# Optimization experiments

Measured on AMD Instinct MI355X. Metric: run time of the kernel, lower is better.

Reference implementation:

```python
import jax, jax.numpy as jnp
import numpy as np
from jax import lax

IN_C, OUT_C, K, Z_DIM, STRIDE = 128, 128, 3, 256, 1


def setup_inputs() -> dict:
    key = jax.random.key(0)
    k1, k2, k3, k4, k5 = jax.random.split(key, 5)
    B, H, W = 16, 64, 64
    x = jax.random.normal(k1, (B, IN_C, H, W), dtype=jnp.float32)
    z = jax.random.normal(k2, (B, Z_DIM), dtype=jnp.float32)
    # base conv weight, He-style init as in the torch module
    base_weight = jax.random.normal(k3, (OUT_C, IN_C, K, K), dtype=jnp.float32) * (2.0 / (IN_C * K * K)) ** 0.5
    # delta_weight_head: nn.Linear(z_dim, out_c*in_c*k*k) -> weight [out_dim, z_dim], bias [out_dim]
    out_dim = OUT_C * IN_C * K * K
    lim = 1.0 / np.sqrt(Z_DIM)
    head_w = jax.random.uniform(k4, (out_dim, Z_DIM), dtype=jnp.float32, minval=-lim, maxval=lim)
    head_b = jax.random.uniform(k5, (out_dim,), dtype=jnp.float32, minval=-lim, maxval=lim)
    return {"x": x, "z": z, "base_weight": base_weight, "head_w": head_w, "head_b": head_b}


def reference(x, z, base_weight, head_w, head_b):
    B = x.shape[0]
    # per-sample weight deltas: [B, out_c*in_c*k*k] -> [B, out_c, in_c, k, k]
    delta_w = (z @ head_w.T + head_b).reshape(B, OUT_C, IN_C, K, K)
    w = base_weight[None] + delta_w  # [B, out_c, in_c, k, k]
    pad = K // 2

    def conv_one(xb, wb):
        # xb: [in_c, H, W], wb: [out_c, in_c, k, k]
        return lax.conv_general_dilated(
            xb[None], wb, window_strides=(STRIDE, STRIDE),
            padding=[(pad, pad), (pad, pad)],
            dimension_numbers=("NCHW", "OIHW", "NCHW"))[0]

    out = jax.vmap(conv_one)(x, w)  # [B, out_c, H_out, W_out]
    return out
```

## Files before the change

### kernel.cpp

```cpp
#include <hip/hip_runtime.h>
#include <cstdint>
#include <cstddef>

typedef _Float16 f16;
typedef _Float16 f16x8 __attribute__((ext_vector_type(8)));
typedef _Float16 f16x4 __attribute__((ext_vector_type(4)));
typedef float f32x4 __attribute__((ext_vector_type(4)));

#define BATCH 16
#define INC   128
#define OUTC  128
#define HH    64
#define WW    64
#define HP    66
#define WP    66
#define ZDIM  256

#define XP_ELEMS (16ull * HP * WP * INC)
#define WA_ELEMS (16ull * 9 * OUTC * INC)

#define GLOAD16(g, l)                                                     \
    __builtin_amdgcn_global_load_lds(                                     \
        (const __attribute__((address_space(1))) void*)(g),               \
        (__attribute__((address_space(3))) void*)(l), 16, 0, 0)

__device__ __forceinline__ f16x8 cvt8(float4 a, float4 b) {
    f16x8 r;
    r[0] = (f16)a.x; r[1] = (f16)a.y; r[2] = (f16)a.z; r[3] = (f16)a.w;
    r[4] = (f16)b.x; r[5] = (f16)b.y; r[6] = (f16)b.z; r[7] = (f16)b.w;
    return r;
}

__global__ __launch_bounds__(256) void prep(const float* __restrict__ x,
                                            const float* __restrict__ z,
                                            const float* __restrict__ base_w,
                                            const float* __restrict__ head_w,
                                            const float* __restrict__ head_b,
                                            f16* __restrict__ xp,
                                            f16* __restrict__ wA) {
    __shared__ float tile[32 * 65];
    int blk = blockIdx.x;
    int tid = threadIdx.x;

    if (blk < 2304) {
        int lane = tid & 63;
        int wv   = tid >> 6;
        int r16  = lane & 15;
        int quad = lane >> 4;
        int tl   = blk * 4 + wv;
        int icb  = tl & 7;
        int oc   = (tl >> 3) & 127;
        int r    = tl >> 10;
        int base = (oc * 128 + icb * 16) * 9 + r;
        int myrow = base + 9 * r16;

        const float4* zrow = (const float4*)(z + (size_t)r16 * ZDIM);
        f16x8 bfr[8];
#pragma unroll
        for (int s = 0; s < 8; ++s)
            bfr[s] = cvt8(zrow[s * 8 + quad * 2], zrow[s * 8 + quad * 2 + 1]);

        const float4* hw = (const float4*)(head_w + (size_t)myrow * ZDIM);
        float4 a[3][2];
        a[0][0] = hw[quad * 2];     a[0][1] = hw[quad * 2 + 1];
        a[1][0] = hw[8 + quad * 2]; a[1][1] = hw[8 + quad * 2 + 1];
        f32x4 acc = {0.f, 0.f, 0.f, 0.f};
#pragma unroll
        for (int s = 0; s < 8; ++s) {
            if (s + 2 < 8) {
                a[(s + 2) % 3][0] = hw[(s + 2) * 8 + quad * 2];
                a[(s + 2) % 3][1] = hw[(s + 2) * 8 + quad * 2 + 1];
            }
            acc = __builtin_amdgcn_mfma_f32_16x16x32_f16(
                cvt8(a[s % 3][0], a[s % 3][1]), bfr[s], acc, 0, 0, 0);
        }

        f16x4 ov;
        int icl = quad * 4;
#pragma unroll
        for (int reg = 0; reg < 4; ++reg) {
            int o = base + 9 * (icl + reg);
            ov[reg] = (f16)(base_w[o] + head_b[o] + acc[reg]);
        }
        size_t idx = (((size_t)r16 * 9 + r) * OUTC + oc) * INC + icb * 16 + icl;
        *(f16x4*)(wA + idx) = ov;

    } else if (blk < 6400) {
        int xb  = blk - 2304;
        int icC = xb & 3;
        int h   = (xb >> 2) & 63;
        int b   = xb >> 8;
        int ic0 = icC * 32;
        {
            int i = tid >> 3;
            int j = tid & 7;
            const float4* src = (const float4*)(x + (((size_t)b * INC + ic0 + i) * HH + h) * WW) + j * 2;
            float4 v0 = src[0];
            float4 v1 = src[1];
            float* tp = tile + i * 65 + j * 8;
            tp[0] = v0.x; tp[1] = v0.y; tp[2] = v0.z; tp[3] = v0.w;
            tp[4] = v1.x; tp[5] = v1.y; tp[6] = v1.z; tp[7] = v1.w;
        }
        __syncthreads();
        {
            int w = tid >> 2;
            int q = tid & 3;
            f16 o8[8];
#pragma unroll
            for (int jj = 0; jj < 8; ++jj)
                o8[jj] = (f16)tile[(q * 8 + jj) * 65 + w];
            f16* dst = xp + (((size_t)b * HP + (h + 1)) * WP + (w + 1)) * INC + ic0 + q * 8;
            *(uint4*)dst = *(uint4*)o8;
        }

    } else {
        unsigned i = (unsigned)(blk - 6400) * 256u + (unsigned)tid;
        unsigned b = i / 4160;
        unsigned j = i - b * 4160;
        unsigned row, wc, ic8;
        if (j < 2112) {
            row = (j < 1056) ? 0u : 65u;
            unsigned jj = (j < 1056) ? j : j - 1056;
            wc  = jj >> 4;
            ic8 = jj & 15;
        } else {
            unsigned j2 = j - 2112;
            row = 1 + (j2 >> 5);
            unsigned k = j2 & 31;
            wc  = (k < 16) ? 0u : 65u;
            ic8 = k & 15;
        }
        uint4 zv = {0u, 0u, 0u, 0u};
        *(uint4*)(xp + (((size_t)b * HP + row) * WP + wc) * INC + ic8 * 8) = zv;
    }
}

__global__ __launch_bounds__(256) void conv(const f16* __restrict__ xp,
                                            const f16* __restrict__ wA,
                                            float* __restrict__ out) {
    int blk0 = blockIdx.x;
    int blk  = (blk0 & 7) * 64 + (blk0 >> 3);
    int b  = blk >> 5;
    int pt = blk & 31;
    int h0 = pt * 2;

    int tid    = threadIdx.x;
    int lane   = tid & 63;
    int wv     = tid >> 6;
    int ocHalf = wv & 1;
    int pHalf  = wv >> 1;
    int m0     = ocHalf * 64;
    int row16  = lane & 15;
    int quad   = lane >> 4;

    __shared__ __align__(16) f16 ws0[3 * 128 * 32];
    __shared__ __align__(16) f16 ws1[3 * 128 * 32];
    __shared__ __align__(16) f16 xs [4 * 66 * 32];

    f32x4 acc[4][4];
#pragma unroll
    for (int mt = 0; mt < 4; ++mt)
#pragma unroll
        for (int nt = 0; nt < 4; ++nt)
            acc[mt][nt] = f32x4{0.f, 0.f, 0.f, 0.f};

    auto stage_w = [&](f16* wb, int c, int kh) {
#pragma unroll
        for (int i = 0; i < 6; ++i) {
            int idx  = tid + i * 256;
            int kw   = idx >> 9;
            int oc   = (idx >> 2) & 127;
            int part = idx & 3;
            const f16* src = wA +
                ((((size_t)b * 9 + kh * 3 + kw) * OUTC + oc) * INC + c * 32 + part * 8);
            GLOAD16(src, wb + (size_t)idx * 8);
        }
    };
    auto stage_x = [&](int c) {
#pragma unroll
        for (int i = 0; i < 5; ++i) {
            int idx = tid + i * 256;
            if (idx < 1056) {
                int seg  = idx >> 2;
                int part = idx & 3;
                int row  = seg / 66;
                int wc   = seg - row * 66;
                const f16* src = xp +
                    ((((size_t)b * HP + h0 + row) * WP + wc) * INC + c * 32 + part * 8);
                GLOAD16(src, xs + (size_t)idx * 8);
            }
        }
    };

    stage_x(0);
    stage_w(ws0, 0, 0);
    __syncthreads();

#pragma unroll
    for (int c = 0; c < 4; ++c) {
#pragma unroll
        for (int kh = 0; kh < 3; ++kh) {
            const int s = c * 3 + kh;
            f16* cur = (s & 1) ? ws1 : ws0;
            if (s < 11) {
                const int sn = s + 1;
                f16* nxt = (sn & 1) ? ws1 : ws0;
                stage_w(nxt, sn / 3, sn % 3);
            }
#pragma unroll
            for (int kw = 0; kw < 3; ++kw) {
                f16x8 afr[4], bfr[4];
#pragma unroll
                for (int mt = 0; mt < 4; ++mt)
                    afr[mt] = *(const f16x8*)(cur +
                        ((size_t)(kw * 128 + m0 + mt * 16 + row16) * 32 + quad * 8));
#pragma unroll
                for (int nt = 0; nt < 4; ++nt)
                    bfr[nt] = *(const f16x8*)(xs +
                        ((size_t)((kh + pHalf) * 66 + nt * 16 + row16 + kw) * 32 + quad * 8));
#pragma unroll
                for (int mt = 0; mt < 4; ++mt)
#pragma unroll
                    for (int nt = 0; nt < 4; ++nt)
                        acc[mt][nt] = __builtin_amdgcn_mfma_f32_16x16x32_f16(
                            afr[mt], bfr[nt], acc[mt][nt], 0, 0, 0);
            }
            __syncthreads();
            if (kh == 2 && c < 3) {
                stage_x(c + 1);
                __syncthreads();
            }
        }
    }

    int hrow = h0 + pHalf;
#pragma unroll
    for (int mt = 0; mt < 4; ++mt)
#pragma unroll
        for (int nt = 0; nt < 4; ++nt) {
            int wc = nt * 16 + row16;
#pragma unroll
            for (int reg = 0; reg < 4; ++reg) {
                int oc = m0 + mt * 16 + quad * 4 + reg;
                out[(((size_t)b * OUTC + oc) * HH + hrow) * WW + wc] = acc[mt][nt][reg];
            }
        }
}

extern "C" void kernel_launch(void* const* d_in, const int* in_sizes, int n_in,
                              void* d_out, int out_size, void* d_ws, size_t ws_size,
                              hipStream_t stream) {
    const float* x      = (const float*)d_in[0];
    const float* z      = (const float*)d_in[1];
    const float* base_w = (const float*)d_in[2];
    const float* head_w = (const float*)d_in[3];
    const float* head_b = (const float*)d_in[4];
    float* out = (float*)d_out;

    f16* xp  = (f16*)d_ws;
    f16* wAp = xp + XP_ELEMS;

    prep<<<6660, 256, 0, stream>>>(x, z, base_w, head_w, head_b, xp, wAp);
    conv<<<512, 256, 0, stream>>>(xp, wAp, out);
}
```

Measured before the change: 276.1 us.

## Prefetch next x chunk into registers and vectorize output stores via swapped MFMA operands

```diff
diff --git a/kernel.cpp b/kernel.cpp
--- a/kernel.cpp
+++ b/kernel.cpp
@@ -159,10 +159,10 @@
 
     f32x4 acc[4][4];
 #pragma unroll
-    for (int mt = 0; mt < 4; ++mt)
-#pragma unroll
-        for (int nt = 0; nt < 4; ++nt)
-            acc[mt][nt] = f32x4{0.f, 0.f, 0.f, 0.f};
+    for (int nt = 0; nt < 4; ++nt)
+#pragma unroll
+        for (int mt = 0; mt < 4; ++mt)
+            acc[nt][mt] = f32x4{0.f, 0.f, 0.f, 0.f};
 
     auto stage_w = [&](f16* wb, int c, int kh) {
 #pragma unroll
@@ -192,6 +192,8 @@
         }
     };
 
+    uint4 xsr[5];
+
     stage_x(0);
     stage_w(ws0, 0, 0);
     __syncthreads();
@@ -207,6 +209,21 @@
                 f16* nxt = (sn & 1) ? ws1 : ws0;
                 stage_w(nxt, sn / 3, sn % 3);
             }
+            if (kh == 1 && c < 3) {
+#pragma unroll
+                for (int i = 0; i < 5; ++i) {
+                    int idx = tid + i * 256;
+                    if (idx < 1056) {
+                        int seg  = idx >> 2;
+                        int part = idx & 3;
+                        int row  = seg / 66;
+                        int wc   = seg - row * 66;
+                        xsr[i] = *(const uint4*)(xp +
+                            ((((size_t)b * HP + h0 + row) * WP + wc) * INC + (c + 1) * 32 + part * 8));
+                    }
+                }
+                __builtin_amdgcn_sched_barrier(0);
+            }
 #pragma unroll
             for (int kw = 0; kw < 3; ++kw) {
                 f16x8 afr[4], bfr[4];
@@ -218,16 +235,23 @@
                 for (int nt = 0; nt < 4; ++nt)
                     bfr[nt] = *(const f16x8*)(xs +
                         ((size_t)((kh + pHalf) * 66 + nt * 16 + row16 + kw) * 32 + quad * 8));
-#pragma unroll
-                for (int mt = 0; mt < 4; ++mt)
-#pragma unroll
-                    for (int nt = 0; nt < 4; ++nt)
-                        acc[mt][nt] = __builtin_amdgcn_mfma_f32_16x16x32_f16(
-                            afr[mt], bfr[nt], acc[mt][nt], 0, 0, 0);
+                __builtin_amdgcn_s_setprio(1);
+#pragma unroll
+                for (int nt = 0; nt < 4; ++nt)
+#pragma unroll
+                    for (int mt = 0; mt < 4; ++mt)
+                        acc[nt][mt] = __builtin_amdgcn_mfma_f32_16x16x32_f16(
+                            bfr[nt], afr[mt], acc[nt][mt], 0, 0, 0);
+                __builtin_amdgcn_s_setprio(0);
             }
             __syncthreads();
             if (kh == 2 && c < 3) {
-                stage_x(c + 1);
+#pragma unroll
+                for (int i = 0; i < 5; ++i) {
+                    int idx = tid + i * 256;
+                    if (idx < 1056)
+                        *(uint4*)(xs + (size_t)idx * 8) = xsr[i];
+                }
                 __syncthreads();
             }
         }
@@ -235,15 +259,12 @@
 
     int hrow = h0 + pHalf;
 #pragma unroll
-    for (int mt = 0; mt < 4; ++mt)
-#pragma unroll
-        for (int nt = 0; nt < 4; ++nt) {
-            int wc = nt * 16 + row16;
-#pragma unroll
-            for (int reg = 0; reg < 4; ++reg) {
-                int oc = m0 + mt * 16 + quad * 4 + reg;
-                out[(((size_t)b * OUTC + oc) * HH + hrow) * WW + wc] = acc[mt][nt][reg];
-            }
+    for (int nt = 0; nt < 4; ++nt)
+#pragma unroll
+        for (int mt = 0; mt < 4; ++mt) {
+            int oc  = m0 + mt * 16 + row16;
+            int wc0 = nt * 16 + quad * 4;
+            *(f32x4*)(out + (((size_t)b * OUTC + oc) * HH + hrow) * WW + wc0) = acc[nt][mt];
         }
 }
 
```

After: 284.2 us. 1.03x slower.
